# Kernel optimization log

Measured on AMD Instinct MI355X. Metric: run time of the kernel, lower is better.

## Reference

```python
import jax, jax.numpy as jnp
import numpy as np

D, NH, NL, NP, DFF = 256, 8, 4, 4, 1024
DH = D // NH
SHAPES = [(64, 64), (32, 32), (16, 16), (8, 8)]
LEN = sum(h * w for h, w in SHAPES)  # 5440
B = 4
EPS = 1e-5


def setup_inputs() -> dict:
    key = jax.random.key(0)
    ks = jax.random.split(key, 24)
    def lin_w(k, fin, fout, scale=None):
        s = (1.0 / np.sqrt(fin)) if scale is None else scale
        return jax.random.normal(k, (fin, fout), jnp.float32) * s
    def lin_b(k, fout, scale=0.01):
        return jax.random.normal(k, (fout,), jnp.float32) * scale
    inp = {
        'src': jax.random.normal(ks[0], (B, LEN, D), jnp.float32),
        'pos_lvl_embed': jax.random.normal(ks[1], (B, LEN, D), jnp.float32),
        'spatial_shapes': jnp.array(SHAPES, jnp.int32),
        'level_start_index': jnp.array(np.cumsum([0] + [h * w for h, w in SHAPES[:-1]]), jnp.int32),
        # MSDeformAttn params
        'Wv': lin_w(ks[2], D, D), 'bv': lin_b(ks[3], D),
        'Woff': lin_w(ks[4], D, NH * NL * NP * 2, scale=0.001),  # small offsets, like grid init
        'boff': jax.random.normal(ks[5], (NH * NL * NP * 2,), jnp.float32) * 0.5,
        'Wa': lin_w(ks[6], D, NH * NL * NP), 'ba': lin_b(ks[7], NH * NL * NP),
        'Wo': lin_w(ks[8], D, D), 'bo': lin_b(ks[9], D),
        # FFN params
        'W1': lin_w(ks[10], D, DFF), 'b1': lin_b(ks[11], DFF),
        'W2': lin_w(ks[12], DFF, D), 'b2': lin_b(ks[13], D),
        # LayerNorms
        'g1': jnp.ones((D,), jnp.float32), 'be1': jnp.zeros((D,), jnp.float32),
        'g2': jnp.ones((D,), jnp.float32), 'be2': jnp.zeros((D,), jnp.float32),
    }
    return inp


def _layernorm(x, g, b):
    mu = jnp.mean(x, axis=-1, keepdims=True)
    var = jnp.var(x, axis=-1, keepdims=True)
    return (x - mu) * jax.lax.rsqrt(var + EPS) * g + b


def _bilinear(v, x, y):
    # v: [B, H, W, NH, DH]; x, y: [B, Lq, NH, NP] pixel coords (align_corners=False, zero padding)
    Bv, H, W = v.shape[0], v.shape[1], v.shape[2]
    x0, y0 = jnp.floor(x), jnp.floor(y)
    bb = jnp.arange(Bv)[:, None, None, None]
    hh = jnp.arange(NH)[None, None, :, None]
    out = 0.0
    for dx in (0, 1):
        for dy in (0, 1):
            xi, yi = x0 + dx, y0 + dy
            w = (1.0 - jnp.abs(x - xi)) * (1.0 - jnp.abs(y - yi))
            valid = (xi >= 0) & (xi <= W - 1) & (yi >= 0) & (yi <= H - 1)
            xc = jnp.clip(xi, 0, W - 1).astype(jnp.int32)
            yc = jnp.clip(yi, 0, H - 1).astype(jnp.int32)
            out = out + v[bb, yc, xc, hh] * (w * valid)[..., None]
    return out  # [B, Lq, NH, NP, DH]


def _ms_deform_attn(query, value_flat, shapes, starts, Wv, bv, Woff, boff, Wa, ba, Wo, bo):
    Bq, Lq = query.shape[0], query.shape[1]
    # reference points: normalized center of each query's own spatial location (valid_ratios == 1)
    refs = []
    for (H, W) in shapes:
        gy, gx = jnp.meshgrid(jnp.arange(H, dtype=jnp.float32), jnp.arange(W, dtype=jnp.float32), indexing='ij')
        refs.append(jnp.stack([(gx + 0.5) / W, (gy + 0.5) / H], -1).reshape(-1, 2))
    ref = jnp.concatenate(refs, 0)  # [Len, 2] (x, y)

    value = (value_flat @ Wv + bv).reshape(Bq, Lq, NH, DH)
    off = (query @ Woff + boff).reshape(Bq, Lq, NH, NL, NP, 2)
    attn = jax.nn.softmax((query @ Wa + ba).reshape(Bq, Lq, NH, NL * NP), axis=-1).reshape(Bq, Lq, NH, NL, NP)
    norm = jnp.array([[w, h] for (h, w) in shapes], jnp.float32)  # [NL, 2] = (W, H)
    loc = ref[None, :, None, None, None, :] + off / norm[None, None, None, :, None, :]  # [B,Lq,NH,NL,NP,2]

    out = 0.0
    for l, (H, W) in enumerate(shapes):
        s = starts[l]
        v_l = value[:, s:s + H * W].reshape(Bq, H, W, NH, DH)
        x = loc[:, :, :, l, :, 0] * W - 0.5
        y = loc[:, :, :, l, :, 1] * H - 0.5
        sampled = _bilinear(v_l, x, y)  # [B,Lq,NH,NP,DH]
        out = out + jnp.sum(sampled * attn[:, :, :, l, :, None], axis=3)
    return out.reshape(Bq, Lq, D) @ Wo + bo


def reference(src, spatial_shapes, level_start_index, pos_lvl_embed,
              Wv, bv, Woff, boff, Wa, ba, Wo, bo,
              W1, b1, W2, b2, g1, be1, g2, be2):
    shapes = [(int(h), int(w)) for h, w in np.asarray(spatial_shapes)]  # static metadata
    starts = [int(s) for s in np.asarray(level_start_index)]
    src2 = _ms_deform_attn(src + pos_lvl_embed, src, shapes, starts, Wv, bv, Woff, boff, Wa, ba, Wo, bo)
    x = _layernorm(src + src2, g1, be1)
    ffn = jax.nn.relu(x @ W1 + b1) @ W2 + b2
    return _layernorm(x + ffn, g2, be2)
```

## Files before the change

kernel.cpp:

```cpp
#include <hip/hip_runtime.h>
#include <hip/hip_fp16.h>
#include <cstddef>
#include <cstdint>

#define DMODEL 256
#define NHEAD  8
#define NLVL   4
#define NPT    4
#define DHEAD  32
#define DFFN   1024
#define SLEN   5440
#define BATCH  4
#define NTOK   (BATCH * SLEN)
#define NT256  ((size_t)NTOK * 256)
#define GYR    170
#define GYP    176
#define LN_EPS 1e-5f

typedef __attribute__((ext_vector_type(4))) float f32x4;
typedef __attribute__((ext_vector_type(8))) short s16x8;

__device__ __forceinline__ unsigned short f2bf(float f) {
    union { float f; unsigned u; } v; v.f = f;
    unsigned u = v.u;
    u += 0x7FFFu + ((u >> 16) & 1u);
    return (unsigned short)(u >> 16);
}
__device__ __forceinline__ float bf2f(unsigned short h) {
    union { unsigned u; float f; } v; v.u = ((unsigned)h) << 16;
    return v.f;
}

__device__ __forceinline__ void g2l16(const unsigned short* g, unsigned short* l) {
    __builtin_amdgcn_global_load_lds(
        (const __attribute__((address_space(1))) unsigned int*)g,
        (__attribute__((address_space(3))) unsigned int*)l, 16, 0, 0);
}

__global__ __launch_bounds__(256) void prep_tr_kernel(
    const float* __restrict__ src, const float* __restrict__ pos,
    unsigned short* __restrict__ srcB, unsigned short* __restrict__ qB,
    const float* __restrict__ Wv, const float* __restrict__ Woff,
    const float* __restrict__ Wa, const float* __restrict__ Wo,
    const float* __restrict__ W1, const float* __restrict__ W2,
    unsigned short* __restrict__ WvT, unsigned short* __restrict__ WcatT,
    unsigned short* __restrict__ WoT,
    unsigned short* __restrict__ W1T, unsigned short* __restrict__ W2T)
{
    if (blockIdx.x < 5440) {
        const size_t i = ((size_t)blockIdx.x * 256 + threadIdx.x) * 4;
        const float4 s = *(const float4*)(src + i);
        const float4 p = *(const float4*)(pos + i);
        ushort4 sb, qb;
        sb.x = f2bf(s.x); sb.y = f2bf(s.y); sb.z = f2bf(s.z); sb.w = f2bf(s.w);
        qb.x = f2bf(s.x + p.x); qb.y = f2bf(s.y + p.y);
        qb.z = f2bf(s.z + p.z); qb.w = f2bf(s.w + p.w);
        *(ushort4*)(srcB + i) = sb;
        *(ushort4*)(qB + i) = qb;
        return;
    }
    const int bid = blockIdx.x - 5440;
    const float* W; unsigned short* Wt; int K, N, t;
    if (bid < 16)       { W = Wv;   Wt = WvT;              K = 256;  N = 256;  t = bid; }
    else if (bid < 32)  { W = Woff; Wt = WcatT;            K = 256;  N = 256;  t = bid - 16; }
    else if (bid < 40)  { W = Wa;   Wt = WcatT + 256*256;  K = 256;  N = 128;  t = bid - 32; }
    else if (bid < 56)  { W = Wo;   Wt = WoT;              K = 256;  N = 256;  t = bid - 40; }
    else if (bid < 120) { W = W1;   Wt = W1T;              K = 256;  N = 1024; t = bid - 56; }
    else                { W = W2;   Wt = W2T;              K = 1024; N = 256;  t = bid - 120; }
    const int ntx = N >> 6;
    const int k0 = (t / ntx) * 64, n0 = (t % ntx) * 64;

    __shared__ float T[64][65];
    const int r  = threadIdx.x >> 4;
    const int c4 = (threadIdx.x & 15) * 4;
    #pragma unroll
    for (int rep = 0; rep < 4; rep++) {
        const int k = rep * 16 + r;
        const float4 v = *(const float4*)(W + (size_t)(k0 + k) * N + n0 + c4);
        T[c4 + 0][k] = v.x; T[c4 + 1][k] = v.y;
        T[c4 + 2][k] = v.z; T[c4 + 3][k] = v.w;
    }
    __syncthreads();
    #pragma unroll
    for (int rep = 0; rep < 4; rep++) {
        const int n = rep * 16 + r;
        ushort4 o;
        o.x = f2bf(T[n][c4 + 0]); o.y = f2bf(T[n][c4 + 1]);
        o.z = f2bf(T[n][c4 + 2]); o.w = f2bf(T[n][c4 + 3]);
        *(ushort4*)(Wt + (size_t)(n0 + n) * K + k0 + c4) = o;
    }
}

template <int KK, int BN, bool RELU, int OM>
__global__ __launch_bounds__(256, 1) void gemm_wide_kernel(
    const unsigned short* __restrict__ A,
    const unsigned short* __restrict__ Bt,
    const float* __restrict__ bias, const float* __restrict__ bias2,
    int bsplit,
    void* __restrict__ Cout)
{
    const int row0 = blockIdx.x * 128;

    __shared__ __align__(16) unsigned short sA[2][128 * 64];
    __shared__ __align__(16) unsigned short sB[2][BN * 64];

    const int tid  = threadIdx.x;
    const int wid  = tid >> 6;
    const int lane = tid & 63;
    const int m16  = lane & 15;
    const int q    = lane >> 4;
    const int wr   = (wid >> 1) * 64;
    const int wc   = (wid & 1) * (BN / 2);

    const int srow = lane >> 3;
    const int schk = (lane & 7) ^ srow;

    constexpr int AI = 4;
    constexpr int BI = BN / 32;
    constexpr int NF = BN / 32;

    auto stage = [&](int buf, int kt) {
        #pragma unroll
        for (int i = 0; i < AI; i++) {
            const int j = wid * AI + i;
            const int r = j * 8 + srow;
            g2l16(A + (size_t)(row0 + r) * KK + kt * 64 + schk * 8,
                  &sA[buf][j * 512]);
        }
        #pragma unroll
        for (int i = 0; i < BI; i++) {
            const int j = wid * BI + i;
            const int r = j * 8 + srow;
            g2l16(Bt + (size_t)r * KK + kt * 64 + schk * 8,
                  &sB[buf][j * 512]);
        }
    };

    f32x4 acc[4][NF];
    #pragma unroll
    for (int m = 0; m < 4; m++)
        #pragma unroll
        for (int n = 0; n < NF; n++) acc[m][n] = (f32x4){0.f, 0.f, 0.f, 0.f};

    constexpr int NT = KK / 64;
    stage(0, 0);
    stage(1, 1);

    #pragma unroll 1
    for (int kt = 0; kt < NT; kt++) {
        const int cur = kt & 1;

        if (kt + 1 < NT) {
            if constexpr (BN == 256) asm volatile("s_waitcnt vmcnt(12)" ::: "memory");
            else                     asm volatile("s_waitcnt vmcnt(16)" ::: "memory");
        } else {
            asm volatile("s_waitcnt vmcnt(0)" ::: "memory");
        }
        __builtin_amdgcn_sched_barrier(0);
        __builtin_amdgcn_s_barrier();
        __builtin_amdgcn_sched_barrier(0);

        #pragma unroll
        for (int ks = 0; ks < 2; ks++) {
            s16x8 a[4], b[NF];
            #pragma unroll
            for (int m = 0; m < 4; m++) {
                const int r  = wr + m * 16 + m16;
                const int cc = (ks * 4 + q) ^ (r & 7);
                a[m] = *(const s16x8*)&sA[cur][r * 64 + cc * 8];
            }
            #pragma unroll
            for (int n = 0; n < NF; n++) {
                const int r  = wc + n * 16 + m16;
                const int cc = (ks * 4 + q) ^ (r & 7);
                b[n] = *(const s16x8*)&sB[cur][r * 64 + cc * 8];
            }
            #pragma unroll
            for (int m = 0; m < 4; m++)
                #pragma unroll
                for (int n = 0; n < NF; n++)
                    acc[m][n] = __builtin_amdgcn_mfma_f32_16x16x32_bf16(
                        a[m], b[n], acc[m][n], 0, 0, 0);
        }

        asm volatile("s_waitcnt lgkmcnt(0)" ::: "memory");
        __builtin_amdgcn_sched_barrier(0);
        __builtin_amdgcn_s_barrier();
        __builtin_amdgcn_sched_barrier(0);

        if (kt + 2 < NT) stage(cur, kt + 2);
    }

    #pragma unroll
    for (int n = 0; n < NF; n++) {
        const int col  = wc + n * 16 + m16;
        const float bc = (col < bsplit) ? bias[col] : bias2[col - bsplit];
        #pragma unroll
        for (int m = 0; m < 4; m++) {
            #pragma unroll
            for (int r = 0; r < 4; r++) {
                const int row = row0 + wr + m * 16 + q * 4 + r;
                float v = acc[m][n][r] + bc;
                if (RELU) v = fmaxf(v, 0.f);
                if (OM == 1)
                    ((unsigned short*)Cout)[(size_t)row * BN + col] = f2bf(v);
                else if (OM == 2)
                    ((__half*)Cout)[(size_t)row * BN + col] = __float2half(v);
                else
                    ((float*)Cout)[(size_t)row * BN + col] = v;
            }
        }
    }
}

template <int KK, int NXB, bool RELU, int OM>
__global__ __launch_bounds__(256, 2) void gemm_lds_kernel(
    const unsigned short* __restrict__ A,
    const unsigned short* __restrict__ Bt,
    const float* __restrict__ bias, const float* __restrict__ bias2,
    int bsplit,
    void* __restrict__ Cout, int N)
{
    const int lin = blockIdx.x;
    const int c8  = lin & 7;
    const int rr  = lin >> 3;
    const int bx  = rr % NXB;
    const int yy  = (rr / NXB) * 8 + c8;
    if (yy >= GYR) return;
    const int row0 = yy * 128;
    const int col0 = bx * 128;

    __shared__ __align__(16) unsigned short sA[2][128 * 64];
    __shared__ __align__(16) unsigned short sB[2][128 * 64];

    const int tid  = threadIdx.x;
    const int wid  = tid >> 6;
    const int lane = tid & 63;
    const int m16  = lane & 15;
    const int q    = lane >> 4;
    const int wr   = (wid >> 1) * 64;
    const int wc   = (wid & 1) * 64;

    const int srow = lane >> 3;
    const int schk = (lane & 7) ^ srow;

    auto stage = [&](int buf, int kt) {
        #pragma unroll
        for (int i = 0; i < 4; i++) {
            const int j = wid * 4 + i;
            const int r = j * 8 + srow;
            g2l16(A  + (size_t)(row0 + r) * KK + kt * 64 + schk * 8,
                  &sA[buf][j * 512]);
            g2l16(Bt + (size_t)(col0 + r) * KK + kt * 64 + schk * 8,
                  &sB[buf][j * 512]);
        }
    };

    f32x4 acc[4][4];
    #pragma unroll
    for (int m = 0; m < 4; m++)
        #pragma unroll
        for (int n = 0; n < 4; n++) acc[m][n] = (f32x4){0.f, 0.f, 0.f, 0.f};

    constexpr int NT = KK / 64;
    stage(0, 0);
    stage(1, 1);

    #pragma unroll 1
    for (int kt = 0; kt < NT; kt++) {
        const int cur = kt & 1;

        if (kt + 1 < NT) asm volatile("s_waitcnt vmcnt(8)" ::: "memory");
        else             asm volatile("s_waitcnt vmcnt(0)" ::: "memory");
        __builtin_amdgcn_sched_barrier(0);
        __builtin_amdgcn_s_barrier();
        __builtin_amdgcn_sched_barrier(0);

        #pragma unroll
        for (int ks = 0; ks < 2; ks++) {
            s16x8 a[4], b[4];
            #pragma unroll
            for (int m = 0; m < 4; m++) {
                const int r  = wr + m * 16 + m16;
                const int cc = (ks * 4 + q) ^ (r & 7);
                a[m] = *(const s16x8*)&sA[cur][r * 64 + cc * 8];
            }
            #pragma unroll
            for (int n = 0; n < 4; n++) {
                const int r  = wc + n * 16 + m16;
                const int cc = (ks * 4 + q) ^ (r & 7);
                b[n] = *(const s16x8*)&sB[cur][r * 64 + cc * 8];
            }
            #pragma unroll
            for (int m = 0; m < 4; m++)
                #pragma unroll
                for (int n = 0; n < 4; n++)
                    acc[m][n] = __builtin_amdgcn_mfma_f32_16x16x32_bf16(
                        a[m], b[n], acc[m][n], 0, 0, 0);
        }

        asm volatile("s_waitcnt lgkmcnt(0)" ::: "memory");
        __builtin_amdgcn_sched_barrier(0);
        __builtin_amdgcn_s_barrier();
        __builtin_amdgcn_sched_barrier(0);

        if (kt + 2 < NT) stage(cur, kt + 2);
    }

    #pragma unroll
    for (int n = 0; n < 4; n++) {
        const int col  = col0 + wc + n * 16 + m16;
        const float bc = (col < bsplit) ? bias[col] : bias2[col - bsplit];
        #pragma unroll
        for (int m = 0; m < 4; m++) {
            #pragma unroll
            for (int r = 0; r < 4; r++) {
                const int row = row0 + wr + m * 16 + q * 4 + r;
                float v = acc[m][n][r] + bc;
                if (RELU) v = fmaxf(v, 0.f);
                if (OM == 1)
                    ((unsigned short*)Cout)[(size_t)row * N + col] = f2bf(v);
                else if (OM == 2)
                    ((__half*)Cout)[(size_t)row * N + col] = __float2half(v);
                else
                    ((float*)Cout)[(size_t)row * N + col] = v;
            }
        }
    }
}

__global__ __launch_bounds__(256) void msda_sample_kernel(
    const __half* __restrict__ value, const float* __restrict__ olg,
    unsigned short* __restrict__ out)
{
    const int lin = blockIdx.x;
    const int c8  = lin & 7;
    const int rr  = lin >> 3;
    const int b   = c8 >> 1;
    const int i8  = (c8 & 1) + 2 * rr;

    const int tid = threadIdx.x;
    const int sub = tid & 3;
    const int h   = (tid >> 2) & 7;
    const int t8  = tid >> 5;
    const int q   = i8 * 8 + t8;
    const int bq  = b * SLEN + q;

    __shared__ __align__(16) uint4 smeta[8 * 16 * 8];

    {
        int rem, Wq;
        if (q < 4096)      { rem = q;        Wq = 64; }
        else if (q < 5120) { rem = q - 4096; Wq = 32; }
        else if (q < 5376) { rem = q - 5120; Wq = 16; }
        else               { rem = q - 5376; Wq = 8;  }
        const int gy = rem / Wq;
        const int gx = rem - gy * Wq;
        const float ref_x = (gx + 0.5f) / (float)Wq;
        const float ref_y = (gy + 0.5f) / (float)Wq;

        const float4 lgv = *(const float4*)(olg + (size_t)bq * 384 + 256 + h * 16 + sub * 4);
        float mx = fmaxf(fmaxf(lgv.x, lgv.y), fmaxf(lgv.z, lgv.w));
        mx = fmaxf(mx, __shfl_xor(mx, 1));
        mx = fmaxf(mx, __shfl_xor(mx, 2));
        float e0 = expf(lgv.x - mx), e1 = expf(lgv.y - mx);
        float e2 = expf(lgv.z - mx), e3 = expf(lgv.w - mx);
        float s = e0 + e1 + e2 + e3;
        s += __shfl_xor(s, 1);
        s += __shfl_xor(s, 2);
        const float inv_s = 1.f / s;

        const float4 o01 = *(const float4*)(olg + (size_t)bq * 384 + h * 32 + sub * 8);
        const float4 o23 = *(const float4*)(olg + (size_t)bq * 384 + h * 32 + sub * 8 + 4);

        constexpr int LW[4] = {64, 32, 16, 8};
        constexpr int LS[4] = {0, 4096, 5120, 5376};
        const int Wl = LW[sub];
        const float fW = (float)Wl;
        const float ew[4] = {e0, e1, e2, e3};
        const float ox[4] = {o01.x, o01.z, o23.x, o23.z};
        const float oy[4] = {o01.y, o01.w, o23.y, o23.w};

        #pragma unroll
        for (int j = 0; j < 4; j++) {
            const float aw = ew[j] * inv_s;
            const float X = (ref_x + ox[j] / fW) * fW - 0.5f;
            const float Y = (ref_y + oy[j] / fW) * fW - 0.5f;
            const float x0f = floorf(X), y0f = floorf(Y);
            const float fx = X - x0f, fy = Y - y0f;
            const int x0 = (int)x0f, y0 = (int)y0f;

            unsigned idx[4]; __half hw[4];
            #pragma unroll
            for (int dy = 0; dy < 2; dy++) {
                const int yi = y0 + dy;
                const float wy = dy ? fy : (1.f - fy);
                const bool vy = (yi >= 0) && (yi < Wl);
                const int yc = min(max(yi, 0), Wl - 1);
                #pragma unroll
                for (int dx = 0; dx < 2; dx++) {
                    const int xi = x0 + dx;
                    const float wx = dx ? fx : (1.f - fx);
                    const bool vx = (xi >= 0) && (xi < Wl);
                    const int xc = min(max(xi, 0), Wl - 1);
                    const int c = dy * 2 + dx;
                    idx[c] = (unsigned)(LS[sub] + yc * Wl + xc);
                    hw[c] = __float2half((vx && vy) ? (aw * wx * wy) : 0.f);
                }
            }
            union { __half2 h2; unsigned u; } pk0, pk1;
            pk0.h2 = __halves2half2(hw[0], hw[1]);
            pk1.h2 = __halves2half2(hw[2], hw[3]);
            uint4 m;
            m.x = idx[0] | (idx[1] << 16);
            m.y = idx[2] | (idx[3] << 16);
            m.z = pk0.u;
            m.w = pk1.u;
            smeta[((t8 * 16) + sub * 4 + j) * 8 + h] = m;
        }
    }
    __syncthreads();

    const char* vb = (const char*)value + (size_t)b * SLEN * 512;
    const unsigned laneoff = (unsigned)(h * 64 + sub * 16);
    const uint4* metap = &smeta[(t8 * 16) * 8 + h];

    __half2 acc[4][4];
    #pragma unroll
    for (int i = 0; i < 4; i++)
        #pragma unroll
        for (int k = 0; k < 4; k++)
            acc[i][k] = __float2half2_rn(0.f);

    for (int g = 0; g < 4; g++) {
        #pragma unroll
        for (int pp = 0; pp < 4; pp++) {
            const int p = g * 4 + pp;
            const uint4 m = metap[p * 8];
            const unsigned a0 = ((m.x & 0xFFFFu) << 9) + laneoff;
            const unsigned a1 = ((m.x >> 16) << 9) + laneoff;
            const unsigned a2 = ((m.y & 0xFFFFu) << 9) + laneoff;
            const unsigned a3 = ((m.y >> 16) << 9) + laneoff;
            const int4 v0 = *(const int4*)(vb + a0);
            const int4 v1 = *(const int4*)(vb + a1);
            const int4 v2 = *(const int4*)(vb + a2);
            const int4 v3 = *(const int4*)(vb + a3);
            union { unsigned u; __half2 h2; } wz, ww;
            wz.u = m.z; ww.u = m.w;
            const __half2 ws0 = __half2half2(__low2half(wz.h2));
            const __half2 ws1 = __half2half2(__high2half(wz.h2));
            const __half2 ws2 = __half2half2(__low2half(ww.h2));
            const __half2 ws3 = __half2half2(__high2half(ww.h2));
            const __half2* p0 = (const __half2*)&v0;
            const __half2* p1 = (const __half2*)&v1;
            const __half2* p2 = (const __half2*)&v2;
            const __half2* p3 = (const __half2*)&v3;
            #pragma unroll
            for (int k = 0; k < 4; k++) {
                acc[pp][k] = __hfma2(ws0, p0[k], acc[pp][k]);
                acc[pp][k] = __hfma2(ws1, p1[k], acc[pp][k]);
                acc[pp][k] = __hfma2(ws2, p2[k], acc[pp][k]);
                acc[pp][k] = __hfma2(ws3, p3[k], acc[pp][k]);
            }
        }
    }

    uint4 o;
    unsigned* ou = &o.x;
    #pragma unroll
    for (int k = 0; k < 4; k++) {
        float2 s = {0.f, 0.f};
        #pragma unroll
        for (int i = 0; i < 4; i++) {
            const float2 f = __half22float2(acc[i][k]);
            s.x += f.x; s.y += f.y;
        }
        ou[k] = (unsigned)f2bf(s.x) | ((unsigned)f2bf(s.y) << 16);
    }
    *(uint4*)(out + (size_t)bq * 256 + h * 32 + sub * 8) = o;
}

template <bool X1B, bool X2B, bool WF, bool WB>
__global__ __launch_bounds__(256) void ln_kernel(
    const void* __restrict__ x1, const void* __restrict__ x2,
    const float* __restrict__ g, const float* __restrict__ be,
    float* __restrict__ outf, unsigned short* __restrict__ outb)
{
    const int lane = threadIdx.x & 63;
    const int wid  = threadIdx.x >> 6;
    const size_t row  = (size_t)blockIdx.x * 4 + wid;
    const size_t base = row * 256 + lane * 4;

    float a0, a1, a2, a3, b0, b1, b2, b3;
    if (X1B) {
        const ushort4 a = *(const ushort4*)((const unsigned short*)x1 + base);
        a0 = bf2f(a.x); a1 = bf2f(a.y); a2 = bf2f(a.z); a3 = bf2f(a.w);
    } else {
        const float4 a = *(const float4*)((const float*)x1 + base);
        a0 = a.x; a1 = a.y; a2 = a.z; a3 = a.w;
    }
    if (X2B) {
        const ushort4 b = *(const ushort4*)((const unsigned short*)x2 + base);
        b0 = bf2f(b.x); b1 = bf2f(b.y); b2 = bf2f(b.z); b3 = bf2f(b.w);
    } else {
        const float4 b = *(const float4*)((const float*)x2 + base);
        b0 = b.x; b1 = b.y; b2 = b.z; b3 = b.w;
    }
    const float v0 = a0 + b0, v1 = a1 + b1, v2 = a2 + b2, v3 = a3 + b3;

    float s  = v0 + v1 + v2 + v3;
    float s2 = v0 * v0 + v1 * v1 + v2 * v2 + v3 * v3;
    #pragma unroll
    for (int o = 32; o > 0; o >>= 1) {
        s  += __shfl_xor(s, o);
        s2 += __shfl_xor(s2, o);
    }
    const float mu  = s * (1.f / 256.f);
    const float var = s2 * (1.f / 256.f) - mu * mu;
    const float r   = rsqrtf(var + LN_EPS);

    const float4 gv = *(const float4*)(g  + lane * 4);
    const float4 bv = *(const float4*)(be + lane * 4);
    float4 o4;
    o4.x = (v0 - mu) * r * gv.x + bv.x;
    o4.y = (v1 - mu) * r * gv.y + bv.y;
    o4.z = (v2 - mu) * r * gv.z + bv.z;
    o4.w = (v3 - mu) * r * gv.w + bv.w;
    if (WF) *(float4*)(outf + base) = o4;
    if (WB) {
        ushort4 ob;
        ob.x = f2bf(o4.x); ob.y = f2bf(o4.y); ob.z = f2bf(o4.z); ob.w = f2bf(o4.w);
        *(ushort4*)(outb + base) = ob;
    }
}

extern "C" void kernel_launch(void* const* d_in, const int* in_sizes, int n_in,
                              void* d_out, int out_size, void* d_ws, size_t ws_size,
                              hipStream_t stream)
{
    const float* src  = (const float*)d_in[0];
    const float* pos  = (const float*)d_in[1];
    const float* Wv   = (const float*)d_in[4];
    const float* bv   = (const float*)d_in[5];
    const float* Woff = (const float*)d_in[6];
    const float* boff = (const float*)d_in[7];
    const float* Wa   = (const float*)d_in[8];
    const float* ba   = (const float*)d_in[9];
    const float* Wo   = (const float*)d_in[10];
    const float* bo   = (const float*)d_in[11];
    const float* W1   = (const float*)d_in[12];
    const float* b1   = (const float*)d_in[13];
    const float* W2   = (const float*)d_in[14];
    const float* b2   = (const float*)d_in[15];
    const float* g1   = (const float*)d_in[16];
    const float* be1  = (const float*)d_in[17];
    const float* g2   = (const float*)d_in[18];
    const float* be2  = (const float*)d_in[19];
    float* out = (float*)d_out;

    char* wsp = (char*)d_ws;
    unsigned short* srcB = (unsigned short*)wsp; wsp += NT256 * 2;
    unsigned short* qB   = (unsigned short*)wsp; wsp += NT256 * 2;
    unsigned short* tbufB = srcB;
    __half*         valB = (__half*)wsp;         wsp += NT256 * 2;
    float*          olg  = (float*)wsp;          wsp += (size_t)NTOK * 384 * 4;
    float*          src2 = olg;
    unsigned short* aoB  = (unsigned short*)wsp; wsp += NT256 * 2;
    unsigned short* xB   = (unsigned short*)wsp; wsp += NT256 * 2;
    unsigned short* h    = (unsigned short*)wsp; wsp += (size_t)NTOK * 1024 * 2;
    unsigned short* WvT  = (unsigned short*)wsp; wsp += 256 * 256 * 2;
    unsigned short* WcatT= (unsigned short*)wsp; wsp += 384 * 256 * 2;
    unsigned short* WoT  = (unsigned short*)wsp; wsp += 256 * 256 * 2;
    unsigned short* W1T  = (unsigned short*)wsp; wsp += 1024 * 256 * 2;
    unsigned short* W2T  = (unsigned short*)wsp; wsp += 256 * 1024 * 2;

    const dim3 blk(256);

    prep_tr_kernel<<<dim3(5624), blk, 0, stream>>>(
        src, pos, srcB, qB, Wv, Woff, Wa, Wo, W1, W2,
        WvT, WcatT, WoT, W1T, W2T);

    gemm_wide_kernel<256, 256, false, 2><<<dim3(GYR), blk, 0, stream>>>(
        srcB, WvT, bv, bv, 1 << 30, valB);
    gemm_wide_kernel<256, 384, false, 0><<<dim3(GYR), blk, 0, stream>>>(
        qB, WcatT, boff, ba, 256, olg);
    msda_sample_kernel<<<dim3(NTOK / 8), blk, 0, stream>>>(valB, olg, aoB);
    gemm_wide_kernel<256, 256, false, 0><<<dim3(GYR), blk, 0, stream>>>(
        aoB, WoT, bo, bo, 1 << 30, src2);
    ln_kernel<false, false, false, true><<<dim3(NTOK / 4), blk, 0, stream>>>(
        src, src2, g1, be1, nullptr, xB);
    gemm_lds_kernel<256, 8, true, 1><<<dim3(8 * GYP), blk, 0, stream>>>(
        xB, W1T, b1, b1, 1 << 30, h, 1024);
    gemm_wide_kernel<1024, 256, false, 1><<<dim3(GYR), blk, 0, stream>>>(
        h, W2T, b2, b2, 1 << 30, tbufB);
    ln_kernel<true, true, true, false><<<dim3(NTOK / 4), blk, 0, stream>>>(
        xB, tbufB, g2, be2, out, nullptr);
}
```

Measured before the change: 259.9 us.

## Fuse residual-add LayerNorm into Wo and W2 GEMM epilogues; retile value/offset GEMMs

Adds a full-row GEMM kernel (128x256 tile) whose epilogue stages the accumulator tile through LDS, adds the residual and applies LayerNorm. This removes two standalone LN kernels and the fp32/bf16 round trip of the intermediate GEMM outputs. The value and offset/attention projections move from the wide 128-row single-block-per-row kernel to the 128x128 tiled kernel with more blocks and two blocks per CU. The fused kernel reuses LDS in two passes with extra barriers, and keeps one block per CU with a large register footprint.

```diff
diff --git a/kernel.cpp b/kernel.cpp
--- a/kernel.cpp
+++ b/kernel.cpp
@@ -91,128 +91,6 @@
     }
 }
 
-template <int KK, int BN, bool RELU, int OM>
-__global__ __launch_bounds__(256, 1) void gemm_wide_kernel(
-    const unsigned short* __restrict__ A,
-    const unsigned short* __restrict__ Bt,
-    const float* __restrict__ bias, const float* __restrict__ bias2,
-    int bsplit,
-    void* __restrict__ Cout)
-{
-    const int row0 = blockIdx.x * 128;
-
-    __shared__ __align__(16) unsigned short sA[2][128 * 64];
-    __shared__ __align__(16) unsigned short sB[2][BN * 64];
-
-    const int tid  = threadIdx.x;
-    const int wid  = tid >> 6;
-    const int lane = tid & 63;
-    const int m16  = lane & 15;
-    const int q    = lane >> 4;
-    const int wr   = (wid >> 1) * 64;
-    const int wc   = (wid & 1) * (BN / 2);
-
-    const int srow = lane >> 3;
-    const int schk = (lane & 7) ^ srow;
-
-    constexpr int AI = 4;
-    constexpr int BI = BN / 32;
-    constexpr int NF = BN / 32;
-
-    auto stage = [&](int buf, int kt) {
-        #pragma unroll
-        for (int i = 0; i < AI; i++) {
-            const int j = wid * AI + i;
-            const int r = j * 8 + srow;
-            g2l16(A + (size_t)(row0 + r) * KK + kt * 64 + schk * 8,
-                  &sA[buf][j * 512]);
-        }
-        #pragma unroll
-        for (int i = 0; i < BI; i++) {
-            const int j = wid * BI + i;
-            const int r = j * 8 + srow;
-            g2l16(Bt + (size_t)r * KK + kt * 64 + schk * 8,
-                  &sB[buf][j * 512]);
-        }
-    };
-
-    f32x4 acc[4][NF];
-    #pragma unroll
-    for (int m = 0; m < 4; m++)
-        #pragma unroll
-        for (int n = 0; n < NF; n++) acc[m][n] = (f32x4){0.f, 0.f, 0.f, 0.f};
-
-    constexpr int NT = KK / 64;
-    stage(0, 0);
-    stage(1, 1);
-
-    #pragma unroll 1
-    for (int kt = 0; kt < NT; kt++) {
-        const int cur = kt & 1;
-
-        if (kt + 1 < NT) {
-            if constexpr (BN == 256) asm volatile("s_waitcnt vmcnt(12)" ::: "memory");
-            else                     asm volatile("s_waitcnt vmcnt(16)" ::: "memory");
-        } else {
-            asm volatile("s_waitcnt vmcnt(0)" ::: "memory");
-        }
-        __builtin_amdgcn_sched_barrier(0);
-        __builtin_amdgcn_s_barrier();
-        __builtin_amdgcn_sched_barrier(0);
-
-        #pragma unroll
-        for (int ks = 0; ks < 2; ks++) {
-            s16x8 a[4], b[NF];
-            #pragma unroll
-            for (int m = 0; m < 4; m++) {
-                const int r  = wr + m * 16 + m16;
-                const int cc = (ks * 4 + q) ^ (r & 7);
-                a[m] = *(const s16x8*)&sA[cur][r * 64 + cc * 8];
-            }
-            #pragma unroll
-            for (int n = 0; n < NF; n++) {
-                const int r  = wc + n * 16 + m16;
-                const int cc = (ks * 4 + q) ^ (r & 7);
-                b[n] = *(const s16x8*)&sB[cur][r * 64 + cc * 8];
-            }
-            #pragma unroll
-            for (int m = 0; m < 4; m++)
-                #pragma unroll
-                for (int n = 0; n < NF; n++)
-                    acc[m][n] = __builtin_amdgcn_mfma_f32_16x16x32_bf16(
-                        a[m], b[n], acc[m][n], 0, 0, 0);
-        }
-
-        asm volatile("s_waitcnt lgkmcnt(0)" ::: "memory");
-        __builtin_amdgcn_sched_barrier(0);
-        __builtin_amdgcn_s_barrier();
-        __builtin_amdgcn_sched_barrier(0);
-
-        if (kt + 2 < NT) stage(cur, kt + 2);
-    }
-
-    #pragma unroll
-    for (int n = 0; n < NF; n++) {
-        const int col  = wc + n * 16 + m16;
-        const float bc = (col < bsplit) ? bias[col] : bias2[col - bsplit];
-        #pragma unroll
-        for (int m = 0; m < 4; m++) {
-            #pragma unroll
-            for (int r = 0; r < 4; r++) {
-                const int row = row0 + wr + m * 16 + q * 4 + r;
-                float v = acc[m][n][r] + bc;
-                if (RELU) v = fmaxf(v, 0.f);
-                if (OM == 1)
-                    ((unsigned short*)Cout)[(size_t)row * BN + col] = f2bf(v);
-                else if (OM == 2)
-                    ((__half*)Cout)[(size_t)row * BN + col] = __float2half(v);
-                else
-                    ((float*)Cout)[(size_t)row * BN + col] = v;
-            }
-        }
-    }
-}
-
 template <int KK, int NXB, bool RELU, int OM>
 __global__ __launch_bounds__(256, 2) void gemm_lds_kernel(
     const unsigned short* __restrict__ A,
@@ -326,6 +204,167 @@
                     ((float*)Cout)[(size_t)row * N + col] = v;
             }
         }
+    }
+}
+
+template <int KK, int LNM>
+__global__ __launch_bounds__(256, 1) void gemm_wide_ln_kernel(
+    const unsigned short* __restrict__ A,
+    const unsigned short* __restrict__ Bt,
+    const float* __restrict__ bias,
+    const void* __restrict__ resid,
+    const float* __restrict__ g, const float* __restrict__ be,
+    void* __restrict__ outp)
+{
+    const int row0 = blockIdx.x * 128;
+
+    __shared__ __align__(16) unsigned short lds[49152];
+
+    const int tid  = threadIdx.x;
+    const int wid  = tid >> 6;
+    const int lane = tid & 63;
+    const int m16  = lane & 15;
+    const int q    = lane >> 4;
+    const int wr   = (wid >> 1) * 64;
+    const int wc   = (wid & 1) * 128;
+
+    const int srow = lane >> 3;
+    const int schk = (lane & 7) ^ srow;
+
+    auto stage = [&](int buf, int kt) {
+        unsigned short* sAb = lds + buf * 8192;
+        unsigned short* sBb = lds + 16384 + buf * 16384;
+        #pragma unroll
+        for (int i = 0; i < 4; i++) {
+            const int j = wid * 4 + i;
+            const int r = j * 8 + srow;
+            g2l16(A + (size_t)(row0 + r) * KK + kt * 64 + schk * 8,
+                  sAb + j * 512);
+        }
+        #pragma unroll
+        for (int i = 0; i < 8; i++) {
+            const int j = wid * 8 + i;
+            const int r = j * 8 + srow;
+            g2l16(Bt + (size_t)r * KK + kt * 64 + schk * 8,
+                  sBb + j * 512);
+        }
+    };
+
+    f32x4 acc[4][8];
+    #pragma unroll
+    for (int m = 0; m < 4; m++)
+        #pragma unroll
+        for (int n = 0; n < 8; n++) acc[m][n] = (f32x4){0.f, 0.f, 0.f, 0.f};
+
+    constexpr int NT = KK / 64;
+    stage(0, 0);
+    stage(1, 1);
+
+    #pragma unroll 1
+    for (int kt = 0; kt < NT; kt++) {
+        const int cur = kt & 1;
+        const unsigned short* sAc = lds + cur * 8192;
+        const unsigned short* sBc = lds + 16384 + cur * 16384;
+
+        if (kt + 1 < NT) asm volatile("s_waitcnt vmcnt(12)" ::: "memory");
+        else             asm volatile("s_waitcnt vmcnt(0)" ::: "memory");
+        __builtin_amdgcn_sched_barrier(0);
+        __builtin_amdgcn_s_barrier();
+        __builtin_amdgcn_sched_barrier(0);
+
+        #pragma unroll
+        for (int ks = 0; ks < 2; ks++) {
+            s16x8 a[4], b[8];
+            #pragma unroll
+            for (int m = 0; m < 4; m++) {
+                const int r  = wr + m * 16 + m16;
+                const int cc = (ks * 4 + q) ^ (r & 7);
+                a[m] = *(const s16x8*)&sAc[r * 64 + cc * 8];
+            }
+            #pragma unroll
+            for (int n = 0; n < 8; n++) {
+                const int r  = wc + n * 16 + m16;
+                const int cc = (ks * 4 + q) ^ (r & 7);
+                b[n] = *(const s16x8*)&sBc[r * 64 + cc * 8];
+            }
+            #pragma unroll
+            for (int m = 0; m < 4; m++)
+                #pragma unroll
+                for (int n = 0; n < 8; n++)
+                    acc[m][n] = __builtin_amdgcn_mfma_f32_16x16x32_bf16(
+                        a[m], b[n], acc[m][n], 0, 0, 0);
+        }
+
+        asm volatile("s_waitcnt lgkmcnt(0)" ::: "memory");
+        __builtin_amdgcn_sched_barrier(0);
+        __builtin_amdgcn_s_barrier();
+        __builtin_amdgcn_sched_barrier(0);
+
+        if (kt + 2 < NT) stage(cur, kt + 2);
+    }
+    float* lnbuf = (float*)lds;
+
+    #pragma unroll 1
+    for (int pass = 0; pass < 2; pass++) {
+        if (wr == pass * 64) {
+            #pragma unroll
+            for (int n = 0; n < 8; n++) {
+                const int col = wc + n * 16 + m16;
+                const float bc = bias[col];
+                #pragma unroll
+                for (int m = 0; m < 4; m++)
+                    #pragma unroll
+                    for (int r = 0; r < 4; r++)
+                        lnbuf[(m * 16 + q * 4 + r) * 260 + col] =
+                            acc[m][n][r] + bc;
+            }
+        }
+        __syncthreads();
+
+        #pragma unroll 1
+        for (int rr2 = 0; rr2 < 16; rr2++) {
+            const int rl = wid * 16 + rr2;
+            const size_t grow = (size_t)row0 + pass * 64 + rl;
+            const size_t base = grow * 256 + lane * 4;
+
+            float4 v = *(const float4*)&lnbuf[rl * 260 + lane * 4];
+            if (LNM == 1) {
+                const float4 rv = *(const float4*)((const float*)resid + base);
+                v.x += rv.x; v.y += rv.y; v.z += rv.z; v.w += rv.w;
+            } else {
+                const ushort4 rb = *(const ushort4*)((const unsigned short*)resid + base);
+                v.x += bf2f(rb.x); v.y += bf2f(rb.y);
+                v.z += bf2f(rb.z); v.w += bf2f(rb.w);
+            }
+
+            float s  = v.x + v.y + v.z + v.w;
+            float s2 = v.x * v.x + v.y * v.y + v.z * v.z + v.w * v.w;
+            #pragma unroll
+            for (int o = 32; o > 0; o >>= 1) {
+                s  += __shfl_xor(s, o);
+                s2 += __shfl_xor(s2, o);
+            }
+            const float mu  = s * (1.f / 256.f);
+            const float var = s2 * (1.f / 256.f) - mu * mu;
+            const float rn  = rsqrtf(var + LN_EPS);
+
+            const float4 gv = *(const float4*)(g  + lane * 4);
+            const float4 bv = *(const float4*)(be + lane * 4);
+            float4 o4;
+            o4.x = (v.x - mu) * rn * gv.x + bv.x;
+            o4.y = (v.y - mu) * rn * gv.y + bv.y;
+            o4.z = (v.z - mu) * rn * gv.z + bv.z;
+            o4.w = (v.w - mu) * rn * gv.w + bv.w;
+            if (LNM == 1) {
+                ushort4 ob;
+                ob.x = f2bf(o4.x); ob.y = f2bf(o4.y);
+                ob.z = f2bf(o4.z); ob.w = f2bf(o4.w);
+                *(ushort4*)((unsigned short*)outp + base) = ob;
+            } else {
+                *(float4*)((float*)outp + base) = o4;
+            }
+        }
+        __syncthreads();
     }
 }
 
@@ -478,60 +517,6 @@
         ou[k] = (unsigned)f2bf(s.x) | ((unsigned)f2bf(s.y) << 16);
     }
     *(uint4*)(out + (size_t)bq * 256 + h * 32 + sub * 8) = o;
-}
-
-template <bool X1B, bool X2B, bool WF, bool WB>
-__global__ __launch_bounds__(256) void ln_kernel(
-    const void* __restrict__ x1, const void* __restrict__ x2,
-    const float* __restrict__ g, const float* __restrict__ be,
-    float* __restrict__ outf, unsigned short* __restrict__ outb)
-{
-    const int lane = threadIdx.x & 63;
-    const int wid  = threadIdx.x >> 6;
-    const size_t row  = (size_t)blockIdx.x * 4 + wid;
-    const size_t base = row * 256 + lane * 4;
-
-    float a0, a1, a2, a3, b0, b1, b2, b3;
-    if (X1B) {
-        const ushort4 a = *(const ushort4*)((const unsigned short*)x1 + base);
-        a0 = bf2f(a.x); a1 = bf2f(a.y); a2 = bf2f(a.z); a3 = bf2f(a.w);
-    } else {
-        const float4 a = *(const float4*)((const float*)x1 + base);
-        a0 = a.x; a1 = a.y; a2 = a.z; a3 = a.w;
-    }
-    if (X2B) {
-        const ushort4 b = *(const ushort4*)((const unsigned short*)x2 + base);
-        b0 = bf2f(b.x); b1 = bf2f(b.y); b2 = bf2f(b.z); b3 = bf2f(b.w);
-    } else {
-        const float4 b = *(const float4*)((const float*)x2 + base);
-        b0 = b.x; b1 = b.y; b2 = b.z; b3 = b.w;
-    }
-    const float v0 = a0 + b0, v1 = a1 + b1, v2 = a2 + b2, v3 = a3 + b3;
-
-    float s  = v0 + v1 + v2 + v3;
-    float s2 = v0 * v0 + v1 * v1 + v2 * v2 + v3 * v3;
-    #pragma unroll
-    for (int o = 32; o > 0; o >>= 1) {
-        s  += __shfl_xor(s, o);
-        s2 += __shfl_xor(s2, o);
-    }
-    const float mu  = s * (1.f / 256.f);
-    const float var = s2 * (1.f / 256.f) - mu * mu;
-    const float r   = rsqrtf(var + LN_EPS);
-
-    const float4 gv = *(const float4*)(g  + lane * 4);
-    const float4 bv = *(const float4*)(be + lane * 4);
-    float4 o4;
-    o4.x = (v0 - mu) * r * gv.x + bv.x;
-    o4.y = (v1 - mu) * r * gv.y + bv.y;
-    o4.z = (v2 - mu) * r * gv.z + bv.z;
-    o4.w = (v3 - mu) * r * gv.w + bv.w;
-    if (WF) *(float4*)(outf + base) = o4;
-    if (WB) {
-        ushort4 ob;
-        ob.x = f2bf(o4.x); ob.y = f2bf(o4.y); ob.z = f2bf(o4.z); ob.w = f2bf(o4.w);
-        *(ushort4*)(outb + base) = ob;
-    }
 }
 
 extern "C" void kernel_launch(void* const* d_in, const int* in_sizes, int n_in,
@@ -561,10 +546,8 @@
     char* wsp = (char*)d_ws;
     unsigned short* srcB = (unsigned short*)wsp; wsp += NT256 * 2;
     unsigned short* qB   = (unsigned short*)wsp; wsp += NT256 * 2;
-    unsigned short* tbufB = srcB;
     __half*         valB = (__half*)wsp;         wsp += NT256 * 2;
     float*          olg  = (float*)wsp;          wsp += (size_t)NTOK * 384 * 4;
-    float*          src2 = olg;
     unsigned short* aoB  = (unsigned short*)wsp; wsp += NT256 * 2;
     unsigned short* xB   = (unsigned short*)wsp; wsp += NT256 * 2;
     unsigned short* h    = (unsigned short*)wsp; wsp += (size_t)NTOK * 1024 * 2;
@@ -580,19 +563,15 @@
         src, pos, srcB, qB, Wv, Woff, Wa, Wo, W1, W2,
         WvT, WcatT, WoT, W1T, W2T);
 
-    gemm_wide_kernel<256, 256, false, 2><<<dim3(GYR), blk, 0, stream>>>(
-        srcB, WvT, bv, bv, 1 << 30, valB);
-    gemm_wide_kernel<256, 384, false, 0><<<dim3(GYR), blk, 0, stream>>>(
-        qB, WcatT, boff, ba, 256, olg);
+    gemm_lds_kernel<256, 2, false, 2><<<dim3(2 * GYP), blk, 0, stream>>>(
+        srcB, WvT, bv, bv, 1 << 30, valB, 256);
+    gemm_lds_kernel<256, 3, false, 0><<<dim3(3 * GYP), blk, 0, stream>>>(
+        qB, WcatT, boff, ba, 256, olg, 384);
     msda_sample_kernel<<<dim3(NTOK / 8), blk, 0, stream>>>(valB, olg, aoB);
-    gemm_wide_kernel<256, 256, false, 0><<<dim3(GYR), blk, 0, stream>>>(
-        aoB, WoT, bo, bo, 1 << 30, src2);
-    ln_kernel<false, false, false, true><<<dim3(NTOK / 4), blk, 0, stream>>>(
-        src, src2, g1, be1, nullptr, xB);
+    gemm_wide_ln_kernel<256, 1><<<dim3(GYR), blk, 0, stream>>>(
+        aoB, WoT, bo, src, g1, be1, xB);
     gemm_lds_kernel<256, 8, true, 1><<<dim3(8 * GYP), blk, 0, stream>>>(
         xB, W1T, b1, b1, 1 << 30, h, 1024);
-    gemm_wide_kernel<1024, 256, false, 1><<<dim3(GYR), blk, 0, stream>>>(
-        h, W2T, b2, b2, 1 << 30, tbufB);
-    ln_kernel<true, true, true, false><<<dim3(NTOK / 4), blk, 0, stream>>>(
-        xB, tbufB, g2, be2, out, nullptr);
-}
+    gemm_wide_ln_kernel<1024, 2><<<dim3(GYR), blk, 0, stream>>>(
+        h, W2T, b2, xB, g2, be2, out);
+}
```

After: 268.2 us. 1.03x slower.
